# Kernel optimization log

Hardware: AMD Instinct MI355X
Metric: run time of the kernel (lower is better)

The kernel has to match this reference:

```python
import jax, jax.numpy as jnp
import numpy as np

V, E, H, K, L = 32000, 512, 512, 512, 4
B, S, T = 128, 49, 16


def setup_inputs() -> dict:
    key = jax.random.key(0)
    ks = jax.random.split(key, 24)
    sd = 0.02
    inp = {
        'features': jax.random.normal(ks[0], (B, S, K), jnp.float32),
        'captions': jax.random.randint(ks[1], (B, T), 0, V),
        'emb': jax.random.normal(ks[2], (V, E), jnp.float32) * sd,
        'fc1_w': jax.random.normal(ks[3], (H, E), jnp.float32) * sd,
        'fc1_b': jnp.zeros((H,), jnp.float32),
        'fc0_w': jax.random.normal(ks[4], (H, K), jnp.float32) * sd,
        'fc0_b': jnp.zeros((H,), jnp.float32),
        'wq': jax.random.normal(ks[5], (H, H), jnp.float32) * sd,
        'bq': jnp.zeros((H,), jnp.float32),
        'wk': jax.random.normal(ks[6], (H, K), jnp.float32) * sd,
        'bk': jnp.zeros((H,), jnp.float32),
        'v_w': jax.random.normal(ks[7], (H,), jnp.float32) * sd,
        'v_b': jnp.zeros((), jnp.float32),
        'gru_wih0': jax.random.normal(ks[8], (3 * H, 2 * H), jnp.float32) * sd,
        'gru_whh0': jax.random.normal(ks[9], (3 * H, H), jnp.float32) * sd,
        'gru_bih0': jnp.zeros((3 * H,), jnp.float32),
        'gru_bhh0': jnp.zeros((3 * H,), jnp.float32),
        'gru_wih_r': jax.random.normal(ks[10], (L - 1, 3 * H, H), jnp.float32) * sd,
        'gru_whh_r': jax.random.normal(ks[11], (L - 1, 3 * H, H), jnp.float32) * sd,
        'gru_bih_r': jnp.zeros((L - 1, 3 * H), jnp.float32),
        'gru_bhh_r': jnp.zeros((L - 1, 3 * H), jnp.float32),
        'fc2_w': jax.random.normal(ks[12], (V, H), jnp.float32) * sd,
        'fc2_b': jnp.zeros((V,), jnp.float32),
    }
    return inp


def _gru_cell(x, h, wih, whh, bih, bhh):
    # torch GRUCell math
    gi = x @ wih.T + bih  # (B, 3H)
    gh = h @ whh.T + bhh
    ir, iz, inn = jnp.split(gi, 3, axis=-1)
    hr, hz, hn = jnp.split(gh, 3, axis=-1)
    r = jax.nn.sigmoid(ir + hr)
    z = jax.nn.sigmoid(iz + hz)
    n = jnp.tanh(inn + r * hn)
    return (1.0 - z) * n + z * h


def reference(features, captions, emb, fc1_w, fc1_b, fc0_w, fc0_b, wq, bq, wk, bk,
              v_w, v_b, gru_wih0, gru_whh0, gru_bih0, gru_bhh0,
              gru_wih_r, gru_whh_r, gru_bih_r, gru_bhh_r, fc2_w, fc2_b):
    # tokens -> x  (B, T, H)
    x = emb[captions] @ fc1_w.T + fc1_b
    keys_proj = features @ wk.T + bk  # (B, S, H), hoisted W_k(keys)

    def step(h, x_t):
        # h: (L, B, H); x_t: (B, H)
        q = h[-1] @ wq.T + bq                                  # (B, H)
        e = jnp.tanh(q[:, None, :] + keys_proj) @ v_w + v_b    # (B, S)
        w = jax.nn.softmax(e, axis=-1)
        context = jnp.einsum('bs,bsk->bk', w, features)        # (B, K)
        ctx = context @ fc0_w.T + fc0_b                        # (B, H)
        rnn_in = jnp.concatenate([x_t, ctx], axis=-1)          # (B, 2H)
        h0 = _gru_cell(rnn_in, h[0], gru_wih0, gru_whh0, gru_bih0, gru_bhh0)
        hs = [h0]
        cur = h0
        for l in range(L - 1):
            cur = _gru_cell(cur, h[l + 1], gru_wih_r[l], gru_whh_r[l],
                            gru_bih_r[l], gru_bhh_r[l])
            hs.append(cur)
        out = cur @ fc2_w.T + fc2_b                            # (B, V)
        return jnp.stack(hs), out

    h0 = jnp.zeros((L, features.shape[0], H), features.dtype)
    xs = jnp.swapaxes(x[:, :T - 1, :], 0, 1)                   # (T-1, B, H)
    _, outs = jax.lax.scan(step, h0, xs)
    return jnp.swapaxes(outs, 0, 1)                            # (B, T-1, V)
```

## Files before the change

kernel.cpp:

```cpp
#include <hip/hip_runtime.h>

typedef __bf16 bf16x8 __attribute__((ext_vector_type(8)));
typedef float  f32x4  __attribute__((ext_vector_type(4)));
typedef unsigned short u16x8 __attribute__((ext_vector_type(8)));
typedef unsigned short u16x4 __attribute__((ext_vector_type(4)));

__device__ __forceinline__ unsigned short f2bf(float f) {
    unsigned int u = __builtin_bit_cast(unsigned int, f);
    unsigned int r = (u + 0x7FFFu + ((u >> 16) & 1u)) >> 16;
    return (unsigned short)r;
}
__device__ __forceinline__ float sigmoid_f(float x) { return 1.f / (1.f + __expf(-x)); }
__device__ __forceinline__ float tanh_f(float x) {
    float e = __expf(2.f * x);
    return 1.f - 2.f / (e + 1.f);
}

template<int BM, int BN, bool A_F32, bool OUT_BF16, bool PERMUTE>
__global__ __launch_bounds__(256) void gemm_bt(
    const void* __restrict__ Aptr, int lda,
    const unsigned short* __restrict__ B, int ldb,
    void* __restrict__ Cptr, int ldc,
    const float* __restrict__ bias, int K)
{
    constexpr int WM = BM / 2, WN = BN / 2;
    constexpr int RM = WM / 16, RN = WN / 16;
    __shared__ unsigned short As[BM][40];
    __shared__ unsigned short Bs[BN][40];
    const int tid = threadIdx.x;
    const int lane = tid & 63, wid = tid >> 6;
    const int wr = wid >> 1, wc = wid & 1;
    const int m0 = blockIdx.y * BM, n0 = blockIdx.x * BN;

    f32x4 acc[RM][RN];
    for (int i = 0; i < RM; i++)
        for (int j = 0; j < RN; j++) acc[i][j] = f32x4{0.f, 0.f, 0.f, 0.f};

    const int nAc = BM * 4;
    const int nBc = BN * 4;
    for (int kt = 0; kt < K; kt += 32) {
        for (int c = tid; c < nAc; c += 256) {
            int r = c >> 2, s = c & 3;
            int kk = kt + s * 8;
            if (A_F32) {
                const float* src = (const float*)Aptr + (size_t)(m0 + r) * lda + kk;
                f32x4 x0 = *(const f32x4*)src;
                f32x4 x1 = *(const f32x4*)(src + 4);
                u16x8 v;
                v[0] = f2bf(x0[0]); v[1] = f2bf(x0[1]); v[2] = f2bf(x0[2]); v[3] = f2bf(x0[3]);
                v[4] = f2bf(x1[0]); v[5] = f2bf(x1[1]); v[6] = f2bf(x1[2]); v[7] = f2bf(x1[3]);
                *(u16x8*)&As[r][s * 8] = v;
            } else {
                const unsigned short* src = (const unsigned short*)Aptr + (size_t)(m0 + r) * lda + kk;
                *(u16x8*)&As[r][s * 8] = *(const u16x8*)src;
            }
        }
        for (int c = tid; c < nBc; c += 256) {
            int r = c >> 2, s = c & 3;
            const unsigned short* src = B + (size_t)(n0 + r) * ldb + kt + s * 8;
            *(u16x8*)&Bs[r][s * 8] = *(const u16x8*)src;
        }
        __syncthreads();
        bf16x8 a[RM], b[RN];
        for (int i = 0; i < RM; i++)
            a[i] = *(const bf16x8*)&As[wr * WM + i * 16 + (lane & 15)][(lane >> 4) * 8];
        for (int j = 0; j < RN; j++)
            b[j] = *(const bf16x8*)&Bs[wc * WN + j * 16 + (lane & 15)][(lane >> 4) * 8];
        for (int i = 0; i < RM; i++)
            for (int j = 0; j < RN; j++)
                acc[i][j] = __builtin_amdgcn_mfma_f32_16x16x32_bf16(a[i], b[j], acc[i][j], 0, 0, 0);
        __syncthreads();
    }
    for (int i = 0; i < RM; i++)
        for (int j = 0; j < RN; j++) {
            int gn = n0 + wc * WN + j * 16 + (lane & 15);
            float bv = bias ? bias[gn] : 0.f;
            for (int rg = 0; rg < 4; rg++) {
                int gm = m0 + wr * WM + i * 16 + (lane >> 4) * 4 + rg;
                float val = acc[i][j][rg] + bv;
                size_t off;
                if (PERMUTE) off = ((size_t)(gm & 127) * 15 + (size_t)(gm >> 7)) * (size_t)ldc + gn;
                else         off = (size_t)gm * (size_t)ldc + gn;
                if (OUT_BF16) ((unsigned short*)Cptr)[off] = f2bf(val);
                else          ((float*)Cptr)[off] = val;
            }
        }
}

__global__ __launch_bounds__(256) void attn_kernel(
    const float* __restrict__ q,
    const float* __restrict__ keys,
    const float* __restrict__ feats,
    const float* __restrict__ vw,
    const float* __restrict__ vb1,
    float* __restrict__ context)
{
    const int b = blockIdx.x;
    const int tid = threadIdx.x;
    const int lane = tid & 63, w = tid >> 6;
    __shared__ float qs[512], vws[512], es[64], wsm[64];
    for (int i = tid; i < 512; i += 256) { qs[i] = q[b * 512 + i]; vws[i] = vw[i]; }
    __syncthreads();
    const float vb = vb1[0];
    for (int s = w; s < 49; s += 4) {
        const float* kp = keys + ((size_t)b * 49 + s) * 512 + lane * 8;
        f32x4 k0 = *(const f32x4*)kp;
        f32x4 k1 = *(const f32x4*)(kp + 4);
        int h0 = lane * 8;
        float acc = 0.f;
        acc += tanh_f(qs[h0 + 0] + k0[0]) * vws[h0 + 0];
        acc += tanh_f(qs[h0 + 1] + k0[1]) * vws[h0 + 1];
        acc += tanh_f(qs[h0 + 2] + k0[2]) * vws[h0 + 2];
        acc += tanh_f(qs[h0 + 3] + k0[3]) * vws[h0 + 3];
        acc += tanh_f(qs[h0 + 4] + k1[0]) * vws[h0 + 4];
        acc += tanh_f(qs[h0 + 5] + k1[1]) * vws[h0 + 5];
        acc += tanh_f(qs[h0 + 6] + k1[2]) * vws[h0 + 6];
        acc += tanh_f(qs[h0 + 7] + k1[3]) * vws[h0 + 7];
        for (int o = 1; o < 64; o <<= 1) acc += __shfl_xor(acc, o, 64);
        if (lane == 0) es[s] = acc + vb;
    }
    __syncthreads();
    if (w == 0) {
        float e = (lane < 49) ? es[lane] : -1e30f;
        float m = e;
        for (int o = 1; o < 64; o <<= 1) m = fmaxf(m, __shfl_xor(m, o, 64));
        float p = (lane < 49) ? __expf(e - m) : 0.f;
        float sum = p;
        for (int o = 1; o < 64; o <<= 1) sum += __shfl_xor(sum, o, 64);
        if (lane < 49) wsm[lane] = p / sum;
    }
    __syncthreads();
    for (int k = tid; k < 512; k += 256) {
        float c = 0.f;
        for (int s = 0; s < 49; s++) c += wsm[s] * feats[((size_t)b * 49 + s) * 512 + k];
        context[(size_t)b * 512 + k] = c;
    }
}

__global__ __launch_bounds__(384) void gru_cell(
    const float* __restrict__ Ax,
    const float* __restrict__ Ah,
    const unsigned short* __restrict__ Bgi,
    const unsigned short* __restrict__ Bgh,
    const float* __restrict__ gi_add, int gi_add_matrix,
    const float* __restrict__ gh_add,
    float* __restrict__ h_out,
    unsigned short* __restrict__ h3_out)
{
    __shared__ unsigned short As[2][32][40];
    __shared__ unsigned short Bs[6][32][40];
    __shared__ float G[6][32][32];
    const int tid = threadIdx.x;
    const int lane = tid & 63, w = tid >> 6;
    const int n0 = blockIdx.x * 32, m0 = blockIdx.y * 32;

    f32x4 acc[2][2];
    acc[0][0] = f32x4{0.f,0.f,0.f,0.f}; acc[0][1] = f32x4{0.f,0.f,0.f,0.f};
    acc[1][0] = f32x4{0.f,0.f,0.f,0.f}; acc[1][1] = f32x4{0.f,0.f,0.f,0.f};

    for (int kt = 0; kt < 512; kt += 32) {
        for (int c = tid; c < 1024; c += 384) {
            if (c < 256) {
                int mi = c >> 7, cc = c & 127;
                int r = cc >> 2, s = cc & 3;
                const float* src = (mi ? Ah : Ax) + (size_t)(m0 + r) * 512 + kt + s * 8;
                f32x4 x0 = *(const f32x4*)src;
                f32x4 x1 = *(const f32x4*)(src + 4);
                u16x8 v;
                v[0] = f2bf(x0[0]); v[1] = f2bf(x0[1]); v[2] = f2bf(x0[2]); v[3] = f2bf(x0[3]);
                v[4] = f2bf(x1[0]); v[5] = f2bf(x1[1]); v[6] = f2bf(x1[2]); v[7] = f2bf(x1[3]);
                *(u16x8*)&As[mi][r][s * 8] = v;
            } else {
                int c2 = c - 256;
                int bi = c2 >> 7, cc = c2 & 127;
                int r = cc >> 2, s = cc & 3;
                int grow = (bi % 3) * 512 + n0 + r;
                const unsigned short* src = (bi < 3 ? Bgi : Bgh) + (size_t)grow * 512 + kt + s * 8;
                *(u16x8*)&Bs[bi][r][s * 8] = *(const u16x8*)src;
            }
        }
        __syncthreads();
        const int ai = (w < 3) ? 0 : 1;
        bf16x8 a0 = *(const bf16x8*)&As[ai][(lane & 15)][(lane >> 4) * 8];
        bf16x8 a1 = *(const bf16x8*)&As[ai][16 + (lane & 15)][(lane >> 4) * 8];
        bf16x8 b0 = *(const bf16x8*)&Bs[w][(lane & 15)][(lane >> 4) * 8];
        bf16x8 b1 = *(const bf16x8*)&Bs[w][16 + (lane & 15)][(lane >> 4) * 8];
        acc[0][0] = __builtin_amdgcn_mfma_f32_16x16x32_bf16(a0, b0, acc[0][0], 0, 0, 0);
        acc[0][1] = __builtin_amdgcn_mfma_f32_16x16x32_bf16(a0, b1, acc[0][1], 0, 0, 0);
        acc[1][0] = __builtin_amdgcn_mfma_f32_16x16x32_bf16(a1, b0, acc[1][0], 0, 0, 0);
        acc[1][1] = __builtin_amdgcn_mfma_f32_16x16x32_bf16(a1, b1, acc[1][1], 0, 0, 0);
        __syncthreads();
    }
    for (int i = 0; i < 2; i++)
        for (int j = 0; j < 2; j++)
            for (int rg = 0; rg < 4; rg++) {
                int row = i * 16 + (lane >> 4) * 4 + rg;
                int col = j * 16 + (lane & 15);
                G[w][row][col] = acc[i][j][rg];
            }
    __syncthreads();
    for (int e = tid; e < 1024; e += 384) {
        int r = e >> 5, c = e & 31;
        int gb = m0 + r, hc = n0 + c;
        float gir, giz, gin;
        if (gi_add_matrix) {
            const float* ga = gi_add + (size_t)gb * 1536;
            gir = G[0][r][c] + ga[hc];
            giz = G[1][r][c] + ga[512 + hc];
            gin = G[2][r][c] + ga[1024 + hc];
        } else {
            gir = G[0][r][c] + gi_add[hc];
            giz = G[1][r][c] + gi_add[512 + hc];
            gin = G[2][r][c] + gi_add[1024 + hc];
        }
        float ghr = G[3][r][c] + gh_add[hc];
        float ghz = G[4][r][c] + gh_add[512 + hc];
        float ghn = G[5][r][c] + gh_add[1024 + hc];
        float rg_ = sigmoid_f(gir + ghr);
        float z   = sigmoid_f(giz + ghz);
        float n   = tanh_f(gin + rg_ * ghn);
        float hp  = Ah[(size_t)gb * 512 + hc];
        float hn  = (1.f - z) * n + z * hp;
        h_out[(size_t)gb * 512 + hc] = hn;
        if (h3_out) h3_out[(size_t)gb * 512 + hc] = f2bf(hn);
    }
}

__global__ void cvt_f32_bf16(const float* __restrict__ s, unsigned short* __restrict__ d, int n4) {
    int i = blockIdx.x * 256 + threadIdx.x;
    if (i >= n4) return;
    f32x4 v = *(const f32x4*)(s + (size_t)i * 4);
    u16x4 o;
    o[0] = f2bf(v[0]); o[1] = f2bf(v[1]); o[2] = f2bf(v[2]); o[3] = f2bf(v[3]);
    *(u16x4*)(d + (size_t)i * 4) = o;
}

__global__ __launch_bounds__(256) void transpose_cvt(const float* __restrict__ src, unsigned short* __restrict__ dst) {
    __shared__ float tile[32][33];
    int bx = blockIdx.x, by = blockIdx.y;
    int lx = threadIdx.x & 31, ly = threadIdx.x >> 5;
    for (int yy = ly; yy < 32; yy += 8)
        tile[yy][lx] = src[(size_t)(by * 32 + yy) * 512 + bx * 32 + lx];
    __syncthreads();
    for (int yy = ly; yy < 32; yy += 8)
        dst[(size_t)(bx * 32 + yy) * 512 + by * 32 + lx] = f2bf(tile[lx][yy]);
}

__global__ __launch_bounds__(256) void bias0_kernel(
    const float* __restrict__ wih0, const float* __restrict__ fc0_b,
    const float* __restrict__ bih0, float* __restrict__ out)
{
    int w = threadIdx.x >> 6, lane = threadIdx.x & 63;
    int i = blockIdx.x * 4 + w;
    const float* row = wih0 + (size_t)i * 1024 + 512;
    float acc = 0.f;
    for (int j = lane; j < 512; j += 64) acc += row[j] * fc0_b[j];
    for (int o = 1; o < 64; o <<= 1) acc += __shfl_xor(acc, o, 64);
    if (lane == 0) out[i] = acc + bih0[i];
}

__global__ void gather_emb(const float* __restrict__ emb, const int* __restrict__ captions,
                           unsigned short* __restrict__ xe) {
    int row = blockIdx.x;
    int t = row >> 7, b = row & 127;
    int tok = captions[b * 16 + t];
    const float* src = emb + (size_t)tok * 512;
    unsigned short* dst = xe + (size_t)row * 512;
    for (int e = threadIdx.x; e < 512; e += blockDim.x) dst[e] = f2bf(src[e]);
}

extern "C" void kernel_launch(void* const* d_in, const int* in_sizes, int n_in,
                              void* d_out, int out_size, void* d_ws, size_t ws_size,
                              hipStream_t stream) {
    const float* features = (const float*)d_in[0];
    const int*   captions = (const int*)d_in[1];
    const float* emb    = (const float*)d_in[2];
    const float* fc1_w  = (const float*)d_in[3];
    const float* fc1_b  = (const float*)d_in[4];
    const float* fc0_w  = (const float*)d_in[5];
    const float* fc0_b  = (const float*)d_in[6];
    const float* wq     = (const float*)d_in[7];
    const float* bq     = (const float*)d_in[8];
    const float* wk     = (const float*)d_in[9];
    const float* bk     = (const float*)d_in[10];
    const float* v_w    = (const float*)d_in[11];
    const float* v_b    = (const float*)d_in[12];
    const float* wih0   = (const float*)d_in[13];
    const float* whh0   = (const float*)d_in[14];
    const float* bih0   = (const float*)d_in[15];
    const float* bhh0   = (const float*)d_in[16];
    const float* wih_r  = (const float*)d_in[17];
    const float* whh_r  = (const float*)d_in[18];
    const float* bih_r  = (const float*)d_in[19];
    const float* bhh_r  = (const float*)d_in[20];
    const float* fc2_w  = (const float*)d_in[21];
    const float* fc2_b  = (const float*)d_in[22];
    float* out = (float*)d_out;

    char* p = (char*)d_ws;
    auto alloc = [&](size_t bytes) { void* r = (void*)p; p += (bytes + 255) & ~(size_t)255; return r; };
    unsigned short* wq_bf   = (unsigned short*)alloc(262144 * 2);
    unsigned short* wk_bf   = (unsigned short*)alloc(262144 * 2);
    unsigned short* fc1_bf  = (unsigned short*)alloc(262144 * 2);
    unsigned short* wih0_bf = (unsigned short*)alloc(1572864 * 2);
    unsigned short* whh0_bf = (unsigned short*)alloc(786432 * 2);
    unsigned short* wihr_bf = (unsigned short*)alloc(2359296 * 2);
    unsigned short* whhr_bf = (unsigned short*)alloc(2359296 * 2);
    unsigned short* fc2_bf  = (unsigned short*)alloc(16384000 * 2);
    unsigned short* fc0T_bf = (unsigned short*)alloc(262144 * 2);
    unsigned short* Wc_bf   = (unsigned short*)alloc(786432 * 2);
    float*          bias0   = (float*)alloc(1536 * 4);
    unsigned short* xe_bf   = (unsigned short*)alloc(983040 * 2);
    unsigned short* x_bf    = (unsigned short*)alloc(983040 * 2);
    float*          gi_x    = (float*)alloc(2949120 * 4);
    float*          keys    = (float*)alloc(3211264 * 4);
    float*          hA      = (float*)alloc(262144 * 4);
    float*          hB      = (float*)alloc(262144 * 4);
    float*          qbuf    = (float*)alloc(65536 * 4);
    float*          ctxbuf  = (float*)alloc(65536 * 4);
    unsigned short* h3all   = (unsigned short*)alloc(983040 * 2);

    hipMemsetAsync(hA, 0, 262144 * 4, stream);

    auto cvt = [&](const float* s, unsigned short* d, int n) {
        int n4 = n / 4;
        cvt_f32_bf16<<<(n4 + 255) / 256, 256, 0, stream>>>(s, d, n4);
    };
    cvt(wq, wq_bf, 262144);
    cvt(wk, wk_bf, 262144);
    cvt(fc1_w, fc1_bf, 262144);
    cvt(wih0, wih0_bf, 1572864);
    cvt(whh0, whh0_bf, 786432);
    cvt(wih_r, wihr_bf, 2359296);
    cvt(whh_r, whhr_bf, 2359296);
    cvt(fc2_w, fc2_bf, 16384000);
    transpose_cvt<<<dim3(16, 16), 256, 0, stream>>>(fc0_w, fc0T_bf);
    bias0_kernel<<<384, 256, 0, stream>>>(wih0, fc0_b, bih0, bias0);
    gather_emb<<<1920, 256, 0, stream>>>(emb, captions, xe_bf);

    gemm_bt<64, 64, false, true, false><<<dim3(8, 30), 256, 0, stream>>>(
        xe_bf, 512, fc1_bf, 512, x_bf, 512, fc1_b, 512);
    gemm_bt<64, 64, false, true, false><<<dim3(8, 24), 256, 0, stream>>>(
        wih0_bf + 512, 1024, fc0T_bf, 512, Wc_bf, 512, nullptr, 512);
    gemm_bt<64, 64, false, false, false><<<dim3(24, 30), 256, 0, stream>>>(
        x_bf, 512, wih0_bf, 1024, gi_x, 1536, bias0, 512);
    gemm_bt<64, 64, true, false, false><<<dim3(8, 98), 256, 0, stream>>>(
        features, 512, wk_bf, 512, keys, 512, bk, 512);

    for (int t = 0; t < 15; t++) {
        float* hold = (t & 1) ? hB : hA;
        float* hnew = (t & 1) ? hA : hB;
        gemm_bt<64, 64, true, false, false><<<dim3(8, 2), 256, 0, stream>>>(
            hold + 3 * 65536, 512, wq_bf, 512, qbuf, 512, bq, 512);
        attn_kernel<<<128, 256, 0, stream>>>(qbuf, keys, features, v_w, v_b, ctxbuf);
        gru_cell<<<dim3(16, 4), 384, 0, stream>>>(
            ctxbuf, hold, Wc_bf, whh0_bf,
            gi_x + (size_t)t * 128 * 1536, 1, bhh0,
            hnew, nullptr);
        for (int l = 1; l < 4; l++) {
            gru_cell<<<dim3(16, 4), 384, 0, stream>>>(
                hnew + (l - 1) * 65536, hold + l * 65536,
                wihr_bf + (size_t)(l - 1) * 786432, whhr_bf + (size_t)(l - 1) * 786432,
                bih_r + (l - 1) * 1536, 0, bhh_r + (l - 1) * 1536,
                hnew + l * 65536,
                (l == 3) ? (h3all + (size_t)t * 65536) : nullptr);
        }
    }
    gemm_bt<128, 128, false, false, true><<<dim3(250, 15), 256, 0, stream>>>(
        h3all, 512, fc2_bf, 512, out, 32000, fc2_b, 512);
}
```

Before: 2.367 ms.

## Fuse decoder time loop into one persistent kernel with grid barriers

Replaces the 75 per-step launches (q GEMM, attention, four GRU cells) with a single persistent kernel of 128 blocks that loops over time and synchronises through a global atomic barrier. Hidden states are also kept as bf16 copies, so the GRU MFMA reads operands straight from global memory without converting in shared memory. The final fc2 GEMM is remapped to a 1D grid that groups N tiles per XCD for L2 locality, and the gemm_bt grid axes are swapped. This removes launch overhead and inter-kernel gaps. In exchange the GRU phases run on only 32 blocks, and correctness depends on all 128 blocks being co-resident.

New measurement: 4.333 ms. +83.1%, slower.

```diff
diff --git a/kernel.cpp b/kernel.cpp
--- a/kernel.cpp
+++ b/kernel.cpp
@@ -10,13 +10,36 @@
     unsigned int r = (u + 0x7FFFu + ((u >> 16) & 1u)) >> 16;
     return (unsigned short)r;
 }
+__device__ __forceinline__ float bfu(unsigned short u) {
+    unsigned int x = (unsigned int)u << 16;
+    return __builtin_bit_cast(float, x);
+}
 __device__ __forceinline__ float sigmoid_f(float x) { return 1.f / (1.f + __expf(-x)); }
 __device__ __forceinline__ float tanh_f(float x) {
     float e = __expf(2.f * x);
     return 1.f - 2.f / (e + 1.f);
 }
 
-template<int BM, int BN, bool A_F32, bool OUT_BF16, bool PERMUTE>
+__device__ __forceinline__ void gsync(unsigned* bar, unsigned nb) {
+    __syncthreads();
+    if (threadIdx.x == 0) {
+        __threadfence();
+        unsigned g = __hip_atomic_load(&bar[1], __ATOMIC_RELAXED, __HIP_MEMORY_SCOPE_AGENT);
+        unsigned old = __hip_atomic_fetch_add(&bar[0], 1u, __ATOMIC_ACQ_REL, __HIP_MEMORY_SCOPE_AGENT);
+        if (old == nb - 1u) {
+            __hip_atomic_store(&bar[0], 0u, __ATOMIC_RELAXED, __HIP_MEMORY_SCOPE_AGENT);
+            __hip_atomic_store(&bar[1], g + 1u, __ATOMIC_RELEASE, __HIP_MEMORY_SCOPE_AGENT);
+        } else {
+            while (__hip_atomic_load(&bar[1], __ATOMIC_ACQUIRE, __HIP_MEMORY_SCOPE_AGENT) == g) {
+                __builtin_amdgcn_s_sleep(2);
+            }
+        }
+        __threadfence();
+    }
+    __syncthreads();
+}
+
+template<int BM, int BN, bool A_F32, bool OUT_BF16, bool PERMUTE, bool XCD1D>
 __global__ __launch_bounds__(256) void gemm_bt(
     const void* __restrict__ Aptr, int lda,
     const unsigned short* __restrict__ B, int ldb,
@@ -30,7 +53,16 @@
     const int tid = threadIdx.x;
     const int lane = tid & 63, wid = tid >> 6;
     const int wr = wid >> 1, wc = wid & 1;
-    const int m0 = blockIdx.y * BM, n0 = blockIdx.x * BN;
+    int m0, n0;
+    if (XCD1D) {
+        int lin = blockIdx.x;
+        int xcd = lin & 7, ix = lin >> 3;
+        int mi = ix % 15, ni = (ix / 15) * 8 + xcd;
+        if (ni >= 250) return;
+        m0 = mi * BM; n0 = ni * BN;
+    } else {
+        m0 = blockIdx.x * BM; n0 = blockIdx.y * BN;
+    }
 
     f32x4 acc[RM][RN];
     for (int i = 0; i < RM; i++)
@@ -87,142 +119,159 @@
         }
 }
 
-__global__ __launch_bounds__(256) void attn_kernel(
-    const float* __restrict__ q,
+#define NBLK 128u
+__global__ __launch_bounds__(512, 2) void decoder_loop(
+    const unsigned short* __restrict__ wq_bf,
+    const float* __restrict__ bq,
     const float* __restrict__ keys,
     const float* __restrict__ feats,
     const float* __restrict__ vw,
     const float* __restrict__ vb1,
-    float* __restrict__ context)
+    const unsigned short* __restrict__ Wc_bf,
+    const unsigned short* __restrict__ whh0_bf,
+    const unsigned short* __restrict__ wihr_bf,
+    const unsigned short* __restrict__ whhr_bf,
+    const float* __restrict__ gi_x,
+    const float* __restrict__ bih_r,
+    const float* __restrict__ bhh0,
+    const float* __restrict__ bhh_r,
+    float* __restrict__ hAf, float* __restrict__ hBf,
+    unsigned short* __restrict__ hAb, unsigned short* __restrict__ hBb,
+    unsigned short* __restrict__ ctx_bf,
+    unsigned short* __restrict__ h3all,
+    unsigned* __restrict__ bar)
 {
-    const int b = blockIdx.x;
+    const int j = blockIdx.x;
     const int tid = threadIdx.x;
     const int lane = tid & 63, w = tid >> 6;
-    __shared__ float qs[512], vws[512], es[64], wsm[64];
-    for (int i = tid; i < 512; i += 256) { qs[i] = q[b * 512 + i]; vws[i] = vw[i]; }
-    __syncthreads();
+    __shared__ __align__(16) unsigned short h3s[512];
+    __shared__ float qs[512];
+    __shared__ float vws[512];
+    __shared__ float es[56], wsm[56];
+    vws[tid & 511] = vw[tid & 511];
     const float vb = vb1[0];
-    for (int s = w; s < 49; s += 4) {
-        const float* kp = keys + ((size_t)b * 49 + s) * 512 + lane * 8;
-        f32x4 k0 = *(const f32x4*)kp;
-        f32x4 k1 = *(const f32x4*)(kp + 4);
-        int h0 = lane * 8;
-        float acc = 0.f;
-        acc += tanh_f(qs[h0 + 0] + k0[0]) * vws[h0 + 0];
-        acc += tanh_f(qs[h0 + 1] + k0[1]) * vws[h0 + 1];
-        acc += tanh_f(qs[h0 + 2] + k0[2]) * vws[h0 + 2];
-        acc += tanh_f(qs[h0 + 3] + k0[3]) * vws[h0 + 3];
-        acc += tanh_f(qs[h0 + 4] + k1[0]) * vws[h0 + 4];
-        acc += tanh_f(qs[h0 + 5] + k1[1]) * vws[h0 + 5];
-        acc += tanh_f(qs[h0 + 6] + k1[2]) * vws[h0 + 6];
-        acc += tanh_f(qs[h0 + 7] + k1[3]) * vws[h0 + 7];
-        for (int o = 1; o < 64; o <<= 1) acc += __shfl_xor(acc, o, 64);
-        if (lane == 0) es[s] = acc + vb;
-    }
-    __syncthreads();
-    if (w == 0) {
-        float e = (lane < 49) ? es[lane] : -1e30f;
-        float m = e;
-        for (int o = 1; o < 64; o <<= 1) m = fmaxf(m, __shfl_xor(m, o, 64));
-        float p = (lane < 49) ? __expf(e - m) : 0.f;
-        float sum = p;
-        for (int o = 1; o < 64; o <<= 1) sum += __shfl_xor(sum, o, 64);
-        if (lane < 49) wsm[lane] = p / sum;
-    }
-    __syncthreads();
-    for (int k = tid; k < 512; k += 256) {
-        float c = 0.f;
-        for (int s = 0; s < 49; s++) c += wsm[s] * feats[((size_t)b * 49 + s) * 512 + k];
-        context[(size_t)b * 512 + k] = c;
-    }
-}
-
-__global__ __launch_bounds__(384) void gru_cell(
-    const float* __restrict__ Ax,
-    const float* __restrict__ Ah,
-    const unsigned short* __restrict__ Bgi,
-    const unsigned short* __restrict__ Bgh,
-    const float* __restrict__ gi_add, int gi_add_matrix,
-    const float* __restrict__ gh_add,
-    float* __restrict__ h_out,
-    unsigned short* __restrict__ h3_out)
-{
-    __shared__ unsigned short As[2][32][40];
-    __shared__ unsigned short Bs[6][32][40];
-    __shared__ float G[6][32][32];
-    const int tid = threadIdx.x;
-    const int lane = tid & 63, w = tid >> 6;
-    const int n0 = blockIdx.x * 32, m0 = blockIdx.y * 32;
-
-    f32x4 acc[2][2];
-    acc[0][0] = f32x4{0.f,0.f,0.f,0.f}; acc[0][1] = f32x4{0.f,0.f,0.f,0.f};
-    acc[1][0] = f32x4{0.f,0.f,0.f,0.f}; acc[1][1] = f32x4{0.f,0.f,0.f,0.f};
-
-    for (int kt = 0; kt < 512; kt += 32) {
-        for (int c = tid; c < 1024; c += 384) {
-            if (c < 256) {
-                int mi = c >> 7, cc = c & 127;
-                int r = cc >> 2, s = cc & 3;
-                const float* src = (mi ? Ah : Ax) + (size_t)(m0 + r) * 512 + kt + s * 8;
-                f32x4 x0 = *(const f32x4*)src;
-                f32x4 x1 = *(const f32x4*)(src + 4);
-                u16x8 v;
-                v[0] = f2bf(x0[0]); v[1] = f2bf(x0[1]); v[2] = f2bf(x0[2]); v[3] = f2bf(x0[3]);
-                v[4] = f2bf(x1[0]); v[5] = f2bf(x1[1]); v[6] = f2bf(x1[2]); v[7] = f2bf(x1[3]);
-                *(u16x8*)&As[mi][r][s * 8] = v;
-            } else {
-                int c2 = c - 256;
-                int bi = c2 >> 7, cc = c2 & 127;
-                int r = cc >> 2, s = cc & 3;
-                int grow = (bi % 3) * 512 + n0 + r;
-                const unsigned short* src = (bi < 3 ? Bgi : Bgh) + (size_t)grow * 512 + kt + s * 8;
-                *(u16x8*)&Bs[bi][r][s * 8] = *(const u16x8*)src;
-            }
-        }
-        __syncthreads();
-        const int ai = (w < 3) ? 0 : 1;
-        bf16x8 a0 = *(const bf16x8*)&As[ai][(lane & 15)][(lane >> 4) * 8];
-        bf16x8 a1 = *(const bf16x8*)&As[ai][16 + (lane & 15)][(lane >> 4) * 8];
-        bf16x8 b0 = *(const bf16x8*)&Bs[w][(lane & 15)][(lane >> 4) * 8];
-        bf16x8 b1 = *(const bf16x8*)&Bs[w][16 + (lane & 15)][(lane >> 4) * 8];
-        acc[0][0] = __builtin_amdgcn_mfma_f32_16x16x32_bf16(a0, b0, acc[0][0], 0, 0, 0);
-        acc[0][1] = __builtin_amdgcn_mfma_f32_16x16x32_bf16(a0, b1, acc[0][1], 0, 0, 0);
-        acc[1][0] = __builtin_amdgcn_mfma_f32_16x16x32_bf16(a1, b0, acc[1][0], 0, 0, 0);
-        acc[1][1] = __builtin_amdgcn_mfma_f32_16x16x32_bf16(a1, b1, acc[1][1], 0, 0, 0);
-        __syncthreads();
-    }
-    for (int i = 0; i < 2; i++)
-        for (int j = 0; j < 2; j++)
-            for (int rg = 0; rg < 4; rg++) {
-                int row = i * 16 + (lane >> 4) * 4 + rg;
-                int col = j * 16 + (lane & 15);
-                G[w][row][col] = acc[i][j][rg];
-            }
-    __syncthreads();
-    for (int e = tid; e < 1024; e += 384) {
-        int r = e >> 5, c = e & 31;
-        int gb = m0 + r, hc = n0 + c;
-        float gir, giz, gin;
-        if (gi_add_matrix) {
-            const float* ga = gi_add + (size_t)gb * 1536;
-            gir = G[0][r][c] + ga[hc];
-            giz = G[1][r][c] + ga[512 + hc];
-            gin = G[2][r][c] + ga[1024 + hc];
-        } else {
-            gir = G[0][r][c] + gi_add[hc];
-            giz = G[1][r][c] + gi_add[512 + hc];
-            gin = G[2][r][c] + gi_add[1024 + hc];
-        }
-        float ghr = G[3][r][c] + gh_add[hc];
-        float ghz = G[4][r][c] + gh_add[512 + hc];
-        float ghn = G[5][r][c] + gh_add[1024 + hc];
-        float rg_ = sigmoid_f(gir + ghr);
-        float z   = sigmoid_f(giz + ghz);
-        float n   = tanh_f(gin + rg_ * ghn);
-        float hp  = Ah[(size_t)gb * 512 + hc];
-        float hn  = (1.f - z) * n + z * hp;
-        h_out[(size_t)gb * 512 + hc] = hn;
-        if (h3_out) h3_out[(size_t)gb * 512 + hc] = f2bf(hn);
+
+    for (int t = 0; t < 15; t++) {
+        const float* hof = (t & 1) ? hBf : hAf;
+        float*       hnf = (t & 1) ? hAf : hBf;
+        const unsigned short* hob = (t & 1) ? hBb : hAb;
+        unsigned short*       hnb = (t & 1) ? hAb : hBb;
+
+        {
+            const int b = j;
+            if (tid < 64) *(u16x8*)&h3s[tid * 8] = *(const u16x8*)(hob + 3 * 65536 + b * 512 + tid * 8);
+            __syncthreads();
+            float qa = bq[tid];
+            const unsigned short* wrow = wq_bf + (size_t)tid * 512;
+            for (int kc = 0; kc < 64; kc++) {
+                u16x8 wv = *(const u16x8*)(wrow + kc * 8);
+                u16x8 hv = *(const u16x8*)&h3s[kc * 8];
+                qa += bfu(wv[0]) * bfu(hv[0]) + bfu(wv[1]) * bfu(hv[1])
+                    + bfu(wv[2]) * bfu(hv[2]) + bfu(wv[3]) * bfu(hv[3])
+                    + bfu(wv[4]) * bfu(hv[4]) + bfu(wv[5]) * bfu(hv[5])
+                    + bfu(wv[6]) * bfu(hv[6]) + bfu(wv[7]) * bfu(hv[7]);
+            }
+            qs[tid] = qa;
+            __syncthreads();
+            for (int s = w; s < 49; s += 8) {
+                const float* kp = keys + ((size_t)b * 49 + s) * 512 + lane * 8;
+                f32x4 k0 = *(const f32x4*)kp;
+                f32x4 k1 = *(const f32x4*)(kp + 4);
+                int h0 = lane * 8;
+                float acc = 0.f;
+                acc += tanh_f(qs[h0 + 0] + k0[0]) * vws[h0 + 0];
+                acc += tanh_f(qs[h0 + 1] + k0[1]) * vws[h0 + 1];
+                acc += tanh_f(qs[h0 + 2] + k0[2]) * vws[h0 + 2];
+                acc += tanh_f(qs[h0 + 3] + k0[3]) * vws[h0 + 3];
+                acc += tanh_f(qs[h0 + 4] + k1[0]) * vws[h0 + 4];
+                acc += tanh_f(qs[h0 + 5] + k1[1]) * vws[h0 + 5];
+                acc += tanh_f(qs[h0 + 6] + k1[2]) * vws[h0 + 6];
+                acc += tanh_f(qs[h0 + 7] + k1[3]) * vws[h0 + 7];
+                for (int o = 1; o < 64; o <<= 1) acc += __shfl_xor(acc, o, 64);
+                if (lane == 0) es[s] = acc + vb;
+            }
+            __syncthreads();
+            if (w == 0) {
+                float e = (lane < 49) ? es[lane] : -1e30f;
+                float m = e;
+                for (int o = 1; o < 64; o <<= 1) m = fmaxf(m, __shfl_xor(m, o, 64));
+                float pp = (lane < 49) ? __expf(e - m) : 0.f;
+                float sum = pp;
+                for (int o = 1; o < 64; o <<= 1) sum += __shfl_xor(sum, o, 64);
+                if (lane < 49) wsm[lane] = pp / sum;
+            }
+            __syncthreads();
+            {
+                const float* fb = feats + (size_t)b * 49 * 512 + tid;
+                float c = 0.f;
+                for (int s = 0; s < 49; s++) c += wsm[s] * fb[s * 512];
+                ctx_bf[b * 512 + tid] = f2bf(c);
+            }
+        }
+        gsync(bar, NBLK);
+
+        for (int c = 0; c < 4; c++) {
+            if (j < 32) {
+                const int n0 = j * 16;
+                const unsigned short* Agi = (c == 0) ? ctx_bf : (hnb + (c - 1) * 65536);
+                const unsigned short* Agh = hob + c * 65536;
+                const unsigned short* Wgi = (c == 0) ? Wc_bf   : (wihr_bf + (size_t)(c - 1) * 786432);
+                const unsigned short* Wgh = (c == 0) ? whh0_bf : (whhr_bf + (size_t)(c - 1) * 786432);
+                const int m0 = w * 16;
+                f32x4 ai[3], ah[3];
+                for (int g = 0; g < 3; g++) { ai[g] = f32x4{0.f,0.f,0.f,0.f}; ah[g] = f32x4{0.f,0.f,0.f,0.f}; }
+                const int arow = m0 + (lane & 15);
+                const int brow = n0 + (lane & 15);
+                const int kk0 = (lane >> 4) * 8;
+                for (int kt = 0; kt < 512; kt += 32) {
+                    bf16x8 a0 = *(const bf16x8*)(Agi + (size_t)arow * 512 + kt + kk0);
+                    bf16x8 a1 = *(const bf16x8*)(Agh + (size_t)arow * 512 + kt + kk0);
+#pragma unroll
+                    for (int g = 0; g < 3; g++) {
+                        bf16x8 b0 = *(const bf16x8*)(Wgi + (size_t)(g * 512 + brow) * 512 + kt + kk0);
+                        bf16x8 b1 = *(const bf16x8*)(Wgh + (size_t)(g * 512 + brow) * 512 + kt + kk0);
+                        ai[g] = __builtin_amdgcn_mfma_f32_16x16x32_bf16(a0, b0, ai[g], 0, 0, 0);
+                        ah[g] = __builtin_amdgcn_mfma_f32_16x16x32_bf16(a1, b1, ah[g], 0, 0, 0);
+                    }
+                }
+                const int col = n0 + (lane & 15);
+                float bir = 0.f, biz = 0.f, bin = 0.f;
+                if (c > 0) {
+                    const float* bi = bih_r + (size_t)(c - 1) * 1536;
+                    bir = bi[col]; biz = bi[512 + col]; bin = bi[1024 + col];
+                }
+                const float* bh = (c == 0) ? bhh0 : (bhh_r + (size_t)(c - 1) * 1536);
+                float bhr = bh[col], bhz = bh[512 + col], bhn = bh[1024 + col];
+#pragma unroll
+                for (int rg = 0; rg < 4; rg++) {
+                    int row = m0 + (lane >> 4) * 4 + rg;
+                    float gir, giz, gin;
+                    if (c == 0) {
+                        const float* gx = gi_x + ((size_t)t * 128 + row) * 1536;
+                        gir = ai[0][rg] + gx[col];
+                        giz = ai[1][rg] + gx[512 + col];
+                        gin = ai[2][rg] + gx[1024 + col];
+                    } else {
+                        gir = ai[0][rg] + bir;
+                        giz = ai[1][rg] + biz;
+                        gin = ai[2][rg] + bin;
+                    }
+                    float ghr = ah[0][rg] + bhr;
+                    float ghz = ah[1][rg] + bhz;
+                    float ghn = ah[2][rg] + bhn;
+                    float r = sigmoid_f(gir + ghr);
+                    float z = sigmoid_f(giz + ghz);
+                    float n = tanh_f(gin + r * ghn);
+                    float hp = hof[c * 65536 + row * 512 + col];
+                    float hv = (1.f - z) * n + z * hp;
+                    hnf[c * 65536 + row * 512 + col] = hv;
+                    unsigned short hb = f2bf(hv);
+                    hnb[c * 65536 + row * 512 + col] = hb;
+                    if (c == 3) h3all[(size_t)t * 65536 + row * 512 + col] = hb;
+                }
+            }
+            gsync(bar, NBLK);
+        }
     }
 }
 
@@ -254,7 +303,7 @@
     int i = blockIdx.x * 4 + w;
     const float* row = wih0 + (size_t)i * 1024 + 512;
     float acc = 0.f;
-    for (int j = lane; j < 512; j += 64) acc += row[j] * fc0_b[j];
+    for (int jj = lane; jj < 512; jj += 64) acc += row[jj] * fc0_b[jj];
     for (int o = 1; o < 64; o <<= 1) acc += __shfl_xor(acc, o, 64);
     if (lane == 0) out[i] = acc + bih0[i];
 }
@@ -314,13 +363,17 @@
     unsigned short* x_bf    = (unsigned short*)alloc(983040 * 2);
     float*          gi_x    = (float*)alloc(2949120 * 4);
     float*          keys    = (float*)alloc(3211264 * 4);
-    float*          hA      = (float*)alloc(262144 * 4);
-    float*          hB      = (float*)alloc(262144 * 4);
-    float*          qbuf    = (float*)alloc(65536 * 4);
-    float*          ctxbuf  = (float*)alloc(65536 * 4);
+    float*          hAf     = (float*)alloc(262144 * 4);
+    float*          hBf     = (float*)alloc(262144 * 4);
+    unsigned short* hAb     = (unsigned short*)alloc(262144 * 2);
+    unsigned short* hBb     = (unsigned short*)alloc(262144 * 2);
+    unsigned short* ctx_bf  = (unsigned short*)alloc(65536 * 2);
     unsigned short* h3all   = (unsigned short*)alloc(983040 * 2);
-
-    hipMemsetAsync(hA, 0, 262144 * 4, stream);
+    unsigned*       bar     = (unsigned*)alloc(256);
+
+    hipMemsetAsync(hAf, 0, 262144 * 4, stream);
+    hipMemsetAsync(hAb, 0, 262144 * 2, stream);
+    hipMemsetAsync(bar, 0, 256, stream);
 
     auto cvt = [&](const float* s, unsigned short* d, int n) {
         int n4 = n / 4;
@@ -338,34 +391,21 @@
     bias0_kernel<<<384, 256, 0, stream>>>(wih0, fc0_b, bih0, bias0);
     gather_emb<<<1920, 256, 0, stream>>>(emb, captions, xe_bf);
 
-    gemm_bt<64, 64, false, true, false><<<dim3(8, 30), 256, 0, stream>>>(
+    gemm_bt<64, 64, false, true, false, false><<<dim3(30, 8), 256, 0, stream>>>(
         xe_bf, 512, fc1_bf, 512, x_bf, 512, fc1_b, 512);
-    gemm_bt<64, 64, false, true, false><<<dim3(8, 24), 256, 0, stream>>>(
+    gemm_bt<64, 64, false, true, false, false><<<dim3(24, 8), 256, 0, stream>>>(
         wih0_bf + 512, 1024, fc0T_bf, 512, Wc_bf, 512, nullptr, 512);
-    gemm_bt<64, 64, false, false, false><<<dim3(24, 30), 256, 0, stream>>>(
+    gemm_bt<64, 64, false, false, false, false><<<dim3(30, 24), 256, 0, stream>>>(
         x_bf, 512, wih0_bf, 1024, gi_x, 1536, bias0, 512);
-    gemm_bt<64, 64, true, false, false><<<dim3(8, 98), 256, 0, stream>>>(
+    gemm_bt<64, 64, true, false, false, false><<<dim3(98, 8), 256, 0, stream>>>(
         features, 512, wk_bf, 512, keys, 512, bk, 512);
 
-    for (int t = 0; t < 15; t++) {
-        float* hold = (t & 1) ? hB : hA;
-        float* hnew = (t & 1) ? hA : hB;
-        gemm_bt<64, 64, true, false, false><<<dim3(8, 2), 256, 0, stream>>>(
-            hold + 3 * 65536, 512, wq_bf, 512, qbuf, 512, bq, 512);
-        attn_kernel<<<128, 256, 0, stream>>>(qbuf, keys, features, v_w, v_b, ctxbuf);
-        gru_cell<<<dim3(16, 4), 384, 0, stream>>>(
-            ctxbuf, hold, Wc_bf, whh0_bf,
-            gi_x + (size_t)t * 128 * 1536, 1, bhh0,
-            hnew, nullptr);
-        for (int l = 1; l < 4; l++) {
-            gru_cell<<<dim3(16, 4), 384, 0, stream>>>(
-                hnew + (l - 1) * 65536, hold + l * 65536,
-                wihr_bf + (size_t)(l - 1) * 786432, whhr_bf + (size_t)(l - 1) * 786432,
-                bih_r + (l - 1) * 1536, 0, bhh_r + (l - 1) * 1536,
-                hnew + l * 65536,
-                (l == 3) ? (h3all + (size_t)t * 65536) : nullptr);
-        }
-    }
-    gemm_bt<128, 128, false, false, true><<<dim3(250, 15), 256, 0, stream>>>(
+    decoder_loop<<<NBLK, 512, 0, stream>>>(
+        wq_bf, bq, keys, features, v_w, v_b,
+        Wc_bf, whh0_bf, wihr_bf, whhr_bf,
+        gi_x, bih_r, bhh0, bhh_r,
+        hAf, hBf, hAb, hBb, ctx_bf, h3all, bar);
+
+    gemm_bt<128, 128, false, false, true, true><<<3840, 256, 0, stream>>>(
         h3all, 512, fc2_bf, 512, out, 32000, fc2_b, 512);
 }
```
